# Optimization experiments

Hardware: AMD Instinct MI355X
Metric: run time of the kernel (lower is better)

The kernel has to match this reference:

```python
import jax, jax.numpy as jnp
import numpy as np

B, P, D, H = 4, 2048, 768, 12  # batch, patches, patch_dims, heads
HD = D // H
EPS = 1e-5


def _layernorm(x, g, b):
    mu = jnp.mean(x, axis=-1, keepdims=True)
    var = jnp.mean(jnp.square(x - mu), axis=-1, keepdims=True)
    return (x - mu) * jax.lax.rsqrt(var + EPS) * g + b


def setup_inputs() -> dict:
    key = jax.random.key(0)
    ks = jax.random.split(key, 4)
    s = 0.02
    return {
        "x": jax.random.normal(ks[0], (B, P, D), jnp.float32),
        "ln1_w": jnp.ones((D,), jnp.float32),
        "ln1_b": jnp.zeros((D,), jnp.float32),
        "w_qkv": jax.random.normal(ks[1], (D, 3 * D), jnp.float32) * s,
        "b_qkv": jnp.zeros((3 * D,), jnp.float32),
        "ln2_w": jnp.ones((D,), jnp.float32),
        "ln2_b": jnp.zeros((D,), jnp.float32),
        "w_fc1": jax.random.normal(ks[2], (D, 4 * D), jnp.float32) * s,
        "b_fc1": jnp.zeros((4 * D,), jnp.float32),
        "w_fc2": jax.random.normal(ks[3], (4 * D, D), jnp.float32) * s,
        "b_fc2": jnp.zeros((D,), jnp.float32),
    }


def reference(x, ln1_w, ln1_b, w_qkv, b_qkv, ln2_w, ln2_b, w_fc1, b_fc1, w_fc2, b_fc2):
    scale = HD ** -0.5
    # --- attention block (pre-norm) ---
    residual = x
    h = _layernorm(x, ln1_w, ln1_b)
    qkv = h @ w_qkv + b_qkv                              # (B, P, 3D)
    qkv = qkv.reshape(B, P, 3, H, HD).transpose(2, 0, 3, 1, 4)  # (3, B, H, P, HD)
    q, k, v = qkv[0], qkv[1], qkv[2]
    attn = jnp.einsum('bhpd,bhqd->bhpq', q, k) * scale   # (B, H, P, P)
    # NOTE: original uses nn.Softmax(dim=1) -> normalizes over HEADS axis
    attn = jax.nn.softmax(attn, axis=1)
    out = jnp.einsum('bhpq,bhqd->bhpd', attn, v)         # (B, H, P, HD)
    out = out.transpose(0, 2, 1, 3).reshape(B, P, D)
    x = out + residual
    # --- MLP block (pre-norm) ---
    residual = x
    h = _layernorm(x, ln2_w, ln2_b)
    h = jax.nn.gelu(h @ w_fc1 + b_fc1, approximate=False)
    h = h @ w_fc2 + b_fc2
    return h + residual
```

## Files before the change

kernel.cpp:

```cpp
#include <hip/hip_runtime.h>
#include <hip/hip_bf16.h>

typedef __bf16 bf8 __attribute__((ext_vector_type(8)));
typedef float f4 __attribute__((ext_vector_type(4)));
typedef unsigned short u16;
typedef unsigned int u32;

#define B_ 4
#define P_ 2048
#define D_ 768
#define H_ 12
#define HD_ 64
#define EXPC_ 0.18033688011112042f

typedef const __attribute__((address_space(1))) void gvoid;
typedef __attribute__((address_space(3))) void lvoid;

__device__ __forceinline__ void gl_lds16(const u16* g, u16* l) {
  __builtin_amdgcn_global_load_lds((gvoid*)g, (lvoid*)l, 16, 0, 0);
}

__device__ __forceinline__ u16 f2bf(float f) {
  union { float f; u32 u; } c; c.f = f;
  u32 u = c.u;
  u += 0x7fffu + ((u >> 16) & 1u);
  return (u16)(u >> 16);
}

__device__ __forceinline__ float bf2f(u16 v) {
  union { u32 u; float f; } c; c.u = (u32)v << 16; return c.f;
}

__device__ __forceinline__ uint2 pack4(f4 v) {
  union { float f; u32 u; } a, b, c, d;
  a.f = v[0]; b.f = v[1]; c.f = v[2]; d.f = v[3];
  uint2 r;
  r.x = (a.u >> 16) | (b.u & 0xffff0000u);
  r.y = (c.u >> 16) | (d.u & 0xffff0000u);
  return r;
}

__device__ __forceinline__ f4 unpack4(ushort4 v) {
  f4 r;
  r[0] = bf2f(v.x); r[1] = bf2f(v.y); r[2] = bf2f(v.z); r[3] = bf2f(v.w);
  return r;
}

__device__ __forceinline__ f4 unp2(uint2 u) {
  f4 r;
  r[0] = bf2f((u16)(u.x & 0xffffu)); r[1] = bf2f((u16)(u.x >> 16));
  r[2] = bf2f((u16)(u.y & 0xffffu)); r[3] = bf2f((u16)(u.y >> 16));
  return r;
}

__device__ __forceinline__ bf8 mkbf8(f4 a, f4 b) {
  union { uint4 u; bf8 v; } c;
  uint2 l = pack4(a), h = pack4(b);
  c.u = make_uint4(l.x, l.y, h.x, h.y);
  return c.v;
}

__device__ __forceinline__ f4 mfma16(bf8 a, bf8 b, f4 c) {
  return __builtin_amdgcn_mfma_f32_16x16x32_bf16(a, b, c, 0, 0, 0);
}

#define ZERO44(acc)                    \
  {                                    \
    f4 z_ = {0.f, 0.f, 0.f, 0.f};      \
    for (int i_ = 0; i_ < 4; ++i_)     \
      for (int j_ = 0; j_ < 4; ++j_)   \
        acc[i_][j_] = z_;              \
  }

__global__ __launch_bounds__(256) void tcast_k(const float* __restrict__ src,
                                               u16* __restrict__ dst, int R, int C) {
  __shared__ float t[32][33];
  int c0 = blockIdx.x * 32, r0 = blockIdx.y * 32;
  int tx = threadIdx.x & 31, ty = threadIdx.x >> 5;
  #pragma unroll
  for (int i = 0; i < 32; i += 8) {
    int r = r0 + ty + i, c = c0 + tx;
    t[ty + i][tx] = (r < R && c < C) ? src[(size_t)r * C + c] : 0.f;
  }
  __syncthreads();
  #pragma unroll
  for (int i = 0; i < 32; i += 8) {
    int c = c0 + ty + i, r = r0 + tx;
    if (c < C && r < R) dst[(size_t)c * R + r] = f2bf(t[tx][ty + i]);
  }
}

__global__ __launch_bounds__(256) void ln_k(const float* __restrict__ x,
                                            const float* __restrict__ g,
                                            const float* __restrict__ b,
                                            u16* __restrict__ out) {
  int row = blockIdx.x;
  const float* xr = x + (size_t)row * D_;
  float v0 = xr[threadIdx.x], v1 = xr[threadIdx.x + 256], v2 = xr[threadIdx.x + 512];
  float s = v0 + v1 + v2;
  float s2 = v0 * v0 + v1 * v1 + v2 * v2;
  #pragma unroll
  for (int o = 32; o > 0; o >>= 1) {
    s += __shfl_down(s, o, 64);
    s2 += __shfl_down(s2, o, 64);
  }
  __shared__ float a[4], a2[4];
  int wv = threadIdx.x >> 6;
  if ((threadIdx.x & 63) == 0) { a[wv] = s; a2[wv] = s2; }
  __syncthreads();
  s = a[0] + a[1] + a[2] + a[3];
  s2 = a2[0] + a2[1] + a2[2] + a2[3];
  float mean = s * (1.f / 768.f);
  float var = s2 * (1.f / 768.f) - mean * mean;
  float rstd = rsqrtf(var + 1e-5f);
  u16* orow = out + (size_t)row * D_;
  float vv[3] = {v0, v1, v2};
  #pragma unroll
  for (int j = 0; j < 3; ++j) {
    int i = threadIdx.x + j * 256;
    orow[i] = f2bf((vv[j] - mean) * rstd * g[i] + b[i]);
  }
}

__global__ __launch_bounds__(256) void ln2add_k(const float* __restrict__ x,
                                                const u16* __restrict__ O0,
                                                const u16* __restrict__ O1,
                                                const float* __restrict__ g,
                                                const float* __restrict__ b,
                                                float* __restrict__ x2,
                                                u16* __restrict__ out) {
  int row = blockIdx.x;
  const float* xr = x + (size_t)row * D_;
  const u16* o0 = O0 + (size_t)row * D_;
  const u16* o1 = O1 + (size_t)row * D_;
  float vv[3];
  #pragma unroll
  for (int j = 0; j < 3; ++j) {
    int i = threadIdx.x + j * 256;
    vv[j] = xr[i] + bf2f(o0[i]) + bf2f(o1[i]);
  }
  float s = vv[0] + vv[1] + vv[2];
  float s2 = vv[0] * vv[0] + vv[1] * vv[1] + vv[2] * vv[2];
  #pragma unroll
  for (int o = 32; o > 0; o >>= 1) {
    s += __shfl_down(s, o, 64);
    s2 += __shfl_down(s2, o, 64);
  }
  __shared__ float a[4], a2[4];
  int wv = threadIdx.x >> 6;
  if ((threadIdx.x & 63) == 0) { a[wv] = s; a2[wv] = s2; }
  __syncthreads();
  s = a[0] + a[1] + a[2] + a[3];
  s2 = a2[0] + a2[1] + a2[2] + a2[3];
  float mean = s * (1.f / 768.f);
  float var = s2 * (1.f / 768.f) - mean * mean;
  float rstd = rsqrtf(var + 1e-5f);
  float* x2r = x2 + (size_t)row * D_;
  u16* orow = out + (size_t)row * D_;
  #pragma unroll
  for (int j = 0; j < 3; ++j) {
    int i = threadIdx.x + j * 256;
    x2r[i] = vv[j];
    orow[i] = f2bf((vv[j] - mean) * rstd * g[i] + b[i]);
  }
}

template <int K>
__device__ __forceinline__ void staged_core(const u16* __restrict__ Ab,
                                            const u16* __restrict__ Bb,
                                            u16* As, u16* Bs, f4 acc[4][4]) {
  const int wave = threadIdx.x >> 6, lane = threadIdx.x & 63;
  const int l15 = lane & 15, quad = lane >> 4;
  const int lrow = lane >> 2;
  const int lcol = (lane & 3) * 8;
  const int mw = (wave & 1) * 64, nw = (wave >> 1) * 64;
  for (int k0 = 0; k0 < K; k0 += 32) {
    const u16* ga = Ab + (size_t)(wave * 32 + lrow) * K + k0 + lcol;
    gl_lds16(ga, &As[(wave * 32) * 32]);
    gl_lds16(ga + (size_t)16 * K, &As[(wave * 32 + 16) * 32]);
    const u16* gb = Bb + (size_t)(wave * 32 + lrow) * K + k0 + lcol;
    gl_lds16(gb, &Bs[(wave * 32) * 32]);
    gl_lds16(gb + (size_t)16 * K, &Bs[(wave * 32 + 16) * 32]);
    __syncthreads();
    bf8 a[4], b[4];
    #pragma unroll
    for (int mt = 0; mt < 4; ++mt)
      a[mt] = *reinterpret_cast<const bf8*>(&As[(mw + mt * 16 + l15) * 32 + quad * 8]);
    #pragma unroll
    for (int nt = 0; nt < 4; ++nt)
      b[nt] = *reinterpret_cast<const bf8*>(&Bs[(nw + nt * 16 + l15) * 32 + quad * 8]);
    #pragma unroll
    for (int mt = 0; mt < 4; ++mt)
      #pragma unroll
      for (int nt = 0; nt < 4; ++nt)
        acc[mt][nt] = mfma16(a[mt], b[nt], acc[mt][nt]);
    __syncthreads();
  }
}

__global__ __launch_bounds__(256) void gemm_qkv_k(const u16* __restrict__ hln,
                                                  const u16* __restrict__ wT,
                                                  const float* __restrict__ bias,
                                                  u16* __restrict__ Q, u16* __restrict__ Km,
                                                  u16* __restrict__ Vt) {
  __shared__ u16 As[128 * 32], Bs[128 * 32];
  int m0 = blockIdx.y * 128, n0 = blockIdx.x * 128;
  f4 acc[4][4];
  ZERO44(acc);
  staged_core<768>(hln + (size_t)m0 * 768, wT + (size_t)n0 * 768, As, Bs, acc);
  int wave = threadIdx.x >> 6, lane = threadIdx.x & 63, l15 = lane & 15, quad = lane >> 4;
  int mW = m0 + (wave & 1) * 64, nW = n0 + (wave >> 1) * 64;
  #pragma unroll
  for (int mt = 0; mt < 4; ++mt)
    #pragma unroll
    for (int nt = 0; nt < 4; ++nt)
      #pragma unroll
      for (int r = 0; r < 4; ++r) {
        int m = mW + mt * 16 + quad * 4 + r;
        int n = nW + nt * 16 + l15;
        float v = acc[mt][nt][r] + bias[n];
        u16 bv = f2bf(v);
        int b = m >> 11, p = m & 2047;
        int which = n / 768, hn = n % 768;
        int h = hn >> 6, d = hn & 63;
        if (which == 0)
          Q[((size_t)(b * H_ + h) * P_ + p) * HD_ + d] = bv;
        else if (which == 1)
          Km[((size_t)(b * H_ + h) * P_ + p) * HD_ + d] = bv;
        else
          Vt[((size_t)(b * H_ + h) * HD_ + d) * P_ + p] = bv;
      }
}

__global__ __launch_bounds__(256) void gemm_fc1_k(const u16* __restrict__ A,
                                                  const u16* __restrict__ wT,
                                                  const float* __restrict__ bias,
                                                  u16* __restrict__ out) {
  __shared__ u16 As[128 * 32], Bs[128 * 32];
  int m0 = blockIdx.y * 128, n0 = blockIdx.x * 128;
  f4 acc[4][4];
  ZERO44(acc);
  staged_core<768>(A + (size_t)m0 * 768, wT + (size_t)n0 * 768, As, Bs, acc);
  int wave = threadIdx.x >> 6, lane = threadIdx.x & 63, l15 = lane & 15, quad = lane >> 4;
  int mW = m0 + (wave & 1) * 64, nW = n0 + (wave >> 1) * 64;
  #pragma unroll
  for (int mt = 0; mt < 4; ++mt)
    #pragma unroll
    for (int nt = 0; nt < 4; ++nt)
      #pragma unroll
      for (int r = 0; r < 4; ++r) {
        int m = mW + mt * 16 + quad * 4 + r;
        int n = nW + nt * 16 + l15;
        float v = acc[mt][nt][r] + bias[n];
        v = 0.5f * v * (1.f + erff(v * 0.70710678f));
        out[(size_t)m * 3072 + n] = f2bf(v);
      }
}

__global__ __launch_bounds__(256) void gemm_fc2_k(const u16* __restrict__ A,
                                                  const u16* __restrict__ wT,
                                                  const float* __restrict__ bias,
                                                  const float* __restrict__ resid,
                                                  float* __restrict__ out) {
  __shared__ u16 As[128 * 32], Bs[64 * 32];
  int wave = threadIdx.x >> 6, lane = threadIdx.x & 63, l15 = lane & 15, quad = lane >> 4;
  int lrow = lane >> 2, lcol = (lane & 3) * 8;
  int m0 = blockIdx.y * 128, n0 = blockIdx.x * 64;
  const u16* Ab = A + (size_t)m0 * 3072;
  const u16* Bb = wT + (size_t)n0 * 3072;
  int mw = (wave & 1) * 64, nw = (wave >> 1) * 32;
  f4 acc[4][2];
  #pragma unroll
  for (int i = 0; i < 4; ++i)
    #pragma unroll
    for (int j = 0; j < 2; ++j) acc[i][j] = f4{0.f, 0.f, 0.f, 0.f};
  for (int k0 = 0; k0 < 3072; k0 += 32) {
    const u16* ga = Ab + (size_t)(wave * 32 + lrow) * 3072 + k0 + lcol;
    gl_lds16(ga, &As[(wave * 32) * 32]);
    gl_lds16(ga + (size_t)16 * 3072, &As[(wave * 32 + 16) * 32]);
    const u16* gb = Bb + (size_t)(wave * 16 + lrow) * 3072 + k0 + lcol;
    gl_lds16(gb, &Bs[(wave * 16) * 32]);
    __syncthreads();
    bf8 a[4], b[2];
    #pragma unroll
    for (int mt = 0; mt < 4; ++mt)
      a[mt] = *reinterpret_cast<const bf8*>(&As[(mw + mt * 16 + l15) * 32 + quad * 8]);
    #pragma unroll
    for (int nt = 0; nt < 2; ++nt)
      b[nt] = *reinterpret_cast<const bf8*>(&Bs[(nw + nt * 16 + l15) * 32 + quad * 8]);
    #pragma unroll
    for (int mt = 0; mt < 4; ++mt)
      #pragma unroll
      for (int nt = 0; nt < 2; ++nt)
        acc[mt][nt] = mfma16(a[mt], b[nt], acc[mt][nt]);
    __syncthreads();
  }
  int mW = m0 + mw, nW = n0 + nw;
  #pragma unroll
  for (int mt = 0; mt < 4; ++mt)
    #pragma unroll
    for (int nt = 0; nt < 2; ++nt)
      #pragma unroll
      for (int r = 0; r < 4; ++r) {
        int m = mW + mt * 16 + quad * 4 + r;
        int n = nW + nt * 16 + l15;
        size_t idx = (size_t)m * 768 + n;
        out[idx] = acc[mt][nt][r] + bias[n] + resid[idx];
      }
}

__global__ __launch_bounds__(768) void attn_fused_k(const u16* __restrict__ Q,
                                                    const u16* __restrict__ Km,
                                                    const u16* __restrict__ Vt,
                                                    u16* __restrict__ O0,
                                                    u16* __restrict__ O1) {
  int id = blockIdx.x;
  int g = id & 7, pt = id >> 3;
  int b = g >> 1, qs = g & 1;
  int w = threadIdx.x >> 6, lane = threadIdx.x & 63, l15 = lane & 15, quad = lane >> 4;
  __shared__ __align__(16) u16 E[12][64][36];
  __shared__ __align__(16) float R[64][32];

  const u16* Qp = Q + ((size_t)(b * H_ + w) * P_ + pt * 64) * HD_;
  const u16* Kbase = Km + ((size_t)(b * H_ + w) * P_ + qs * 1024) * HD_;
  const u16* Vbase = Vt + (size_t)(b * H_ + w) * HD_ * P_ + qs * 1024;

  bf8 qf[4][2];
  #pragma unroll
  for (int nt = 0; nt < 4; ++nt)
    #pragma unroll
    for (int ks = 0; ks < 2; ++ks)
      qf[nt][ks] = *reinterpret_cast<const bf8*>(Qp + (size_t)(nt * 16 + l15) * HD_ + ks * 32 + quad * 8);

  f4 oacc[4][4];
  ZERO44(oacc);

  for (int qt = 0; qt < 32; ++qt) {
    const u16* Kp = Kbase + (size_t)qt * 32 * HD_;
    bf8 kf[2][2];
    #pragma unroll
    for (int mt = 0; mt < 2; ++mt)
      #pragma unroll
      for (int ks = 0; ks < 2; ++ks)
        kf[mt][ks] = *reinterpret_cast<const bf8*>(Kp + (size_t)(mt * 16 + l15) * HD_ + ks * 32 + quad * 8);
    bf8 vf[4];
    #pragma unroll
    for (int dt = 0; dt < 4; ++dt)
      vf[dt] = *reinterpret_cast<const bf8*>(Vbase + (size_t)(dt * 16 + l15) * P_ + qt * 32 + quad * 8);
    #pragma unroll
    for (int mt = 0; mt < 2; ++mt) {
      f4 s[4];
      #pragma unroll
      for (int nt = 0; nt < 4; ++nt) s[nt] = f4{0.f, 0.f, 0.f, 0.f};
      #pragma unroll
      for (int nt = 0; nt < 4; ++nt) {
        s[nt] = mfma16(kf[mt][0], qf[nt][0], s[nt]);
        s[nt] = mfma16(kf[mt][1], qf[nt][1], s[nt]);
      }
      #pragma unroll
      for (int nt = 0; nt < 4; ++nt) {
        f4 e;
        #pragma unroll
        for (int r = 0; r < 4; ++r) e[r] = __builtin_amdgcn_exp2f(s[nt][r] * EXPC_);
        *reinterpret_cast<uint2*>(&E[w][nt * 16 + l15][mt * 16 + quad * 4]) = pack4(e);
      }
    }
    __syncthreads();
    if (threadIdx.x < 512) {
      int p = threadIdx.x >> 3, qc = (threadIdx.x & 7) * 4;
      f4 sum = {0.f, 0.f, 0.f, 0.f};
      #pragma unroll
      for (int h = 0; h < 12; ++h)
        sum += unpack4(*reinterpret_cast<const ushort4*>(&E[h][p][qc]));
      f4 rc;
      #pragma unroll
      for (int c = 0; c < 4; ++c) rc[c] = __builtin_amdgcn_rcpf(sum[c]);
      *reinterpret_cast<f4*>(&R[p][qc]) = rc;
    }
    __syncthreads();
    #pragma unroll
    for (int pi = 0; pi < 4; ++pi) {
      int pp = pi * 16 + l15;
      uint2 e0 = *reinterpret_cast<const uint2*>(&E[w][pp][quad * 8]);
      uint2 e1 = *reinterpret_cast<const uint2*>(&E[w][pp][quad * 8 + 4]);
      f4 r0 = *reinterpret_cast<const f4*>(&R[pp][quad * 8]);
      f4 r1 = *reinterpret_cast<const f4*>(&R[pp][quad * 8 + 4]);
      bf8 af = mkbf8(unp2(e0) * r0, unp2(e1) * r1);
      #pragma unroll
      for (int dt = 0; dt < 4; ++dt)
        oacc[dt][pi] = mfma16(vf[dt], af, oacc[dt][pi]);
    }
  }
  __syncthreads();
  u16(*Os)[64][72] = reinterpret_cast<u16(*)[64][72]>(&E[0][0][0]);
  u16* Op = qs ? O1 : O0;
  #pragma unroll
  for (int hh = 0; hh < 2; ++hh) {
    if (w >= hh * 6 && w < hh * 6 + 6) {
      int wp = w - hh * 6;
      #pragma unroll
      for (int dt = 0; dt < 4; ++dt)
        #pragma unroll
        for (int pi = 0; pi < 4; ++pi)
          *reinterpret_cast<uint2*>(&Os[wp][pi * 16 + l15][dt * 16 + quad * 4]) = pack4(oacc[dt][pi]);
    }
    __syncthreads();
    #pragma unroll
    for (int j = 0; j < 4; ++j) {
      int c = threadIdx.x + j * 768;
      int p = c / 48, m = c % 48;
      int hp = m >> 3, d = (m & 7) * 8;
      uint4 val = *reinterpret_cast<const uint4*>(&Os[hp][p][d]);
      size_t go = (((size_t)b * P_) + pt * 64 + p) * D_ + (hh * 6 + hp) * 64 + d;
      *reinterpret_cast<uint4*>(Op + go) = val;
    }
    __syncthreads();
  }
}

extern "C" void kernel_launch(void* const* d_in, const int* in_sizes, int n_in,
                              void* d_out, int out_size, void* d_ws, size_t ws_size,
                              hipStream_t stream) {
  const float* x = (const float*)d_in[0];
  const float* ln1w = (const float*)d_in[1];
  const float* ln1b = (const float*)d_in[2];
  const float* wqkv = (const float*)d_in[3];
  const float* bqkv = (const float*)d_in[4];
  const float* ln2w = (const float*)d_in[5];
  const float* ln2b = (const float*)d_in[6];
  const float* wfc1 = (const float*)d_in[7];
  const float* bfc1 = (const float*)d_in[8];
  const float* wfc2 = (const float*)d_in[9];
  const float* bfc2 = (const float*)d_in[10];
  float* out = (float*)d_out;

  char* ws = (char*)d_ws;
  size_t off = 0;
  auto alloc = [&](size_t bytes) -> void* {
    void* p = ws + off;
    off += (bytes + 255) & ~(size_t)255;
    return p;
  };
  u16* hln = (u16*)alloc((size_t)8192 * 768 * 2);
  u16* wqkvT = (u16*)alloc((size_t)2304 * 768 * 2);
  u16* wfc1T = (u16*)alloc((size_t)3072 * 768 * 2);
  u16* wfc2T = (u16*)alloc((size_t)768 * 3072 * 2);
  u16* Qb = (u16*)alloc((size_t)B_ * H_ * P_ * HD_ * 2);
  u16* Kb = (u16*)alloc((size_t)B_ * H_ * P_ * HD_ * 2);
  u16* Vtb = (u16*)alloc((size_t)B_ * H_ * HD_ * P_ * 2);
  float* x2 = (float*)alloc((size_t)8192 * 768 * 4);
  u16* O0 = (u16*)alloc((size_t)8192 * 768 * 2);
  u16* O1 = (u16*)alloc((size_t)8192 * 768 * 2);
  u16* gbuf = (u16*)alloc((size_t)8192 * 3072 * 2);

  tcast_k<<<dim3(72, 24), 256, 0, stream>>>(wqkv, wqkvT, 768, 2304);
  tcast_k<<<dim3(96, 24), 256, 0, stream>>>(wfc1, wfc1T, 768, 3072);
  tcast_k<<<dim3(24, 96), 256, 0, stream>>>(wfc2, wfc2T, 3072, 768);
  ln_k<<<8192, 256, 0, stream>>>(x, ln1w, ln1b, hln);
  gemm_qkv_k<<<dim3(18, 64), 256, 0, stream>>>(hln, wqkvT, bqkv, Qb, Kb, Vtb);
  attn_fused_k<<<256, 768, 0, stream>>>(Qb, Kb, Vtb, O0, O1);
  ln2add_k<<<8192, 256, 0, stream>>>(x, O0, O1, ln2w, ln2b, x2, hln);
  gemm_fc1_k<<<dim3(24, 64), 256, 0, stream>>>(hln, wfc1T, bfc1, gbuf);
  gemm_fc2_k<<<dim3(12, 64), 256, 0, stream>>>(gbuf, wfc2T, bfc2, x2, out);
}
```

Baseline: 481.0 us.

## Software-pipeline attention S-phase with head-sum/PV phase and pad R array

Restructures the attention loop so the QK^T MFMA and exp for the next key tile run in registers while the cross-head sum and PV MFMA of the current tile proceed, with K loads prefetched two tiles ahead. The exp results are written to LDS only after the PV phase, which removes one barrier-separated serial stage per iteration. It also pads the reciprocal array R to 35 columns and switches its accesses to scalar loads and stores to avoid LDS bank conflicts. The pipelining raises register pressure and the scalar R accesses add LDS instructions.

```diff
diff --git a/kernel.cpp b/kernel.cpp
--- a/kernel.cpp
+++ b/kernel.cpp
@@ -319,7 +319,7 @@
   int b = g >> 1, qs = g & 1;
   int w = threadIdx.x >> 6, lane = threadIdx.x & 63, l15 = lane & 15, quad = lane >> 4;
   __shared__ __align__(16) u16 E[12][64][36];
-  __shared__ __align__(16) float R[64][32];
+  __shared__ __align__(16) float R[64][35];
 
   const u16* Qp = Q + ((size_t)(b * H_ + w) * P_ + pt * 64) * HD_;
   const u16* Kbase = Km + ((size_t)(b * H_ + w) * P_ + qs * 1024) * HD_;
@@ -335,47 +335,76 @@
   f4 oacc[4][4];
   ZERO44(oacc);
 
+  bf8 kf[2][2];
+
+#define LOADK(t)                                                                      \
+  {                                                                                   \
+    const u16* Kp_ = Kbase + (size_t)(t) * 32 * HD_;                                  \
+    _Pragma("unroll")                                                                 \
+    for (int mt_ = 0; mt_ < 2; ++mt_)                                                 \
+      _Pragma("unroll")                                                               \
+      for (int ks_ = 0; ks_ < 2; ++ks_)                                               \
+        kf[mt_][ks_] = *reinterpret_cast<const bf8*>(                                 \
+            Kp_ + (size_t)(mt_ * 16 + l15) * HD_ + ks_ * 32 + quad * 8);              \
+  }
+
+#define SPHASE(ereg)                                                                  \
+  {                                                                                   \
+    _Pragma("unroll")                                                                 \
+    for (int mt_ = 0; mt_ < 2; ++mt_) {                                               \
+      f4 s_[4];                                                                       \
+      _Pragma("unroll")                                                               \
+      for (int nt_ = 0; nt_ < 4; ++nt_) s_[nt_] = f4{0.f, 0.f, 0.f, 0.f};             \
+      _Pragma("unroll")                                                               \
+      for (int nt_ = 0; nt_ < 4; ++nt_) {                                             \
+        s_[nt_] = mfma16(kf[mt_][0], qf[nt_][0], s_[nt_]);                            \
+        s_[nt_] = mfma16(kf[mt_][1], qf[nt_][1], s_[nt_]);                            \
+      }                                                                               \
+      _Pragma("unroll")                                                               \
+      for (int nt_ = 0; nt_ < 4; ++nt_) {                                             \
+        f4 e_;                                                                        \
+        _Pragma("unroll")                                                             \
+        for (int r_ = 0; r_ < 4; ++r_) e_[r_] = __builtin_amdgcn_exp2f(s_[nt_][r_] * EXPC_); \
+        ereg[mt_][nt_] = pack4(e_);                                                   \
+      }                                                                               \
+    }                                                                                 \
+  }
+
+#define WRITEE(ereg)                                                                  \
+  {                                                                                   \
+    _Pragma("unroll")                                                                 \
+    for (int mt_ = 0; mt_ < 2; ++mt_)                                                 \
+      _Pragma("unroll")                                                               \
+      for (int nt_ = 0; nt_ < 4; ++nt_)                                               \
+        *reinterpret_cast<uint2*>(&E[w][nt_ * 16 + l15][mt_ * 16 + quad * 4]) =       \
+            ereg[mt_][nt_];                                                           \
+  }
+
+  LOADK(0);
+  {
+    uint2 er[2][4];
+    SPHASE(er);
+    WRITEE(er);
+  }
+  LOADK(1);
+
   for (int qt = 0; qt < 32; ++qt) {
-    const u16* Kp = Kbase + (size_t)qt * 32 * HD_;
-    bf8 kf[2][2];
-    #pragma unroll
-    for (int mt = 0; mt < 2; ++mt)
-      #pragma unroll
-      for (int ks = 0; ks < 2; ++ks)
-        kf[mt][ks] = *reinterpret_cast<const bf8*>(Kp + (size_t)(mt * 16 + l15) * HD_ + ks * 32 + quad * 8);
+    __syncthreads();
     bf8 vf[4];
     #pragma unroll
     for (int dt = 0; dt < 4; ++dt)
       vf[dt] = *reinterpret_cast<const bf8*>(Vbase + (size_t)(dt * 16 + l15) * P_ + qt * 32 + quad * 8);
-    #pragma unroll
-    for (int mt = 0; mt < 2; ++mt) {
-      f4 s[4];
-      #pragma unroll
-      for (int nt = 0; nt < 4; ++nt) s[nt] = f4{0.f, 0.f, 0.f, 0.f};
-      #pragma unroll
-      for (int nt = 0; nt < 4; ++nt) {
-        s[nt] = mfma16(kf[mt][0], qf[nt][0], s[nt]);
-        s[nt] = mfma16(kf[mt][1], qf[nt][1], s[nt]);
-      }
-      #pragma unroll
-      for (int nt = 0; nt < 4; ++nt) {
-        f4 e;
-        #pragma unroll
-        for (int r = 0; r < 4; ++r) e[r] = __builtin_amdgcn_exp2f(s[nt][r] * EXPC_);
-        *reinterpret_cast<uint2*>(&E[w][nt * 16 + l15][mt * 16 + quad * 4]) = pack4(e);
-      }
-    }
-    __syncthreads();
+    uint2 ereg[2][4];
+    if (qt < 31) SPHASE(ereg);
     if (threadIdx.x < 512) {
       int p = threadIdx.x >> 3, qc = (threadIdx.x & 7) * 4;
       f4 sum = {0.f, 0.f, 0.f, 0.f};
       #pragma unroll
       for (int h = 0; h < 12; ++h)
         sum += unpack4(*reinterpret_cast<const ushort4*>(&E[h][p][qc]));
-      f4 rc;
-      #pragma unroll
-      for (int c = 0; c < 4; ++c) rc[c] = __builtin_amdgcn_rcpf(sum[c]);
-      *reinterpret_cast<f4*>(&R[p][qc]) = rc;
+      float* Rr = &R[p][qc];
+      #pragma unroll
+      for (int c = 0; c < 4; ++c) Rr[c] = __builtin_amdgcn_rcpf(sum[c]);
     }
     __syncthreads();
     #pragma unroll
@@ -383,12 +412,18 @@
       int pp = pi * 16 + l15;
       uint2 e0 = *reinterpret_cast<const uint2*>(&E[w][pp][quad * 8]);
       uint2 e1 = *reinterpret_cast<const uint2*>(&E[w][pp][quad * 8 + 4]);
-      f4 r0 = *reinterpret_cast<const f4*>(&R[pp][quad * 8]);
-      f4 r1 = *reinterpret_cast<const f4*>(&R[pp][quad * 8 + 4]);
+      const float* Rr = &R[pp][quad * 8];
+      f4 r0, r1;
+      r0[0] = Rr[0]; r0[1] = Rr[1]; r0[2] = Rr[2]; r0[3] = Rr[3];
+      r1[0] = Rr[4]; r1[1] = Rr[5]; r1[2] = Rr[6]; r1[3] = Rr[7];
       bf8 af = mkbf8(unp2(e0) * r0, unp2(e1) * r1);
       #pragma unroll
       for (int dt = 0; dt < 4; ++dt)
         oacc[dt][pi] = mfma16(vf[dt], af, oacc[dt][pi]);
+    }
+    if (qt < 31) {
+      WRITEE(ereg);
+      if (qt < 30) LOADK(qt + 2);
     }
   }
   __syncthreads();
@@ -416,6 +451,9 @@
     }
     __syncthreads();
   }
+#undef LOADK
+#undef SPHASE
+#undef WRITEE
 }
 
 extern "C" void kernel_launch(void* const* d_in, const int* in_sizes, int n_in,
```

After: 506.3 us. 5.2% more time.
